# Optimization experiments

Hardware: AMD Instinct MI355X
Metric: run time of the kernel (lower is better)

The kernel has to match this reference:

```python
import jax, jax.numpy as jnp
import numpy as np

D_K = 128
D_V = 128
SEQ_LEN = 2048


def setup_inputs() -> dict:
    key = jax.random.key(0)
    kq, kk, kv = jax.random.split(key, 3)
    q = jax.random.normal(kq, (SEQ_LEN, D_K), dtype=jnp.float32)
    k = jax.random.normal(kk, (SEQ_LEN, D_K), dtype=jnp.float32)
    v = jax.random.normal(kv, (SEQ_LEN, D_V), dtype=jnp.float32)
    return {"q": q, "k": k, "v": v}


def _step(carry, qkv):
    J, Svv, Sqv, Sqq, l = carry
    q, k, v = qkv
    l = l + 1
    fl = l.astype(J.dtype)
    # update_correlations: running means of outer products
    Svv = (fl - 1.0) / fl * Svv + jnp.outer(v, v) / fl
    Sqv = (fl - 1.0) / fl * Sqv + jnp.outer(q, v) / fl
    Sqq = (fl - 1.0) / fl * Sqq + jnp.outer(q, q) / fl

    first = l == 1

    # ecological params (J: [d_v, d_k], Sqv: [d_k, d_v], Sqq: [d_k, d_k])
    s_J = jnp.einsum('vk,kv->', J, Sqv)            # trace(J @ Sigma_qv)
    s_l = k @ Sqv @ v
    A_JJ = jnp.einsum('vk,kj,vj->', J, Sqq, J)     # trace(J Sqq J^T)
    A_ll = (v @ v) * (k @ Sqq @ k)
    A_Jl = v @ J @ Sqq @ k

    # safe denominators (unused branches must not produce NaN under where)
    A_JJ_s = jnp.where(first | (A_JJ == 0), 1.0, A_JJ)
    A_ll_s = jnp.where(first | (A_ll == 0), 1.0, A_ll)
    denom = A_JJ * A_ll - A_Jl ** 2
    denom_s = jnp.where(first | (denom == 0), 1.0, denom)

    margin = s_l - A_Jl * (s_J / A_JJ_s)

    wf = (A_ll * s_J - A_Jl * s_l) / denom_s
    wi = (A_JJ * s_l - A_Jl * s_J) / denom_s
    # nonnegativity constraints (check omega_i first, as in the source)
    wf_c = jnp.where(wi <= 0, s_J / A_JJ_s, jnp.where(wf <= 0, 0.0, wf))
    wi_c = jnp.where(wi <= 0, 0.0, jnp.where(wf <= 0, s_l / A_ll_s, wi))

    do_update = margin > 0
    vk = jnp.outer(v, k)
    J_upd = jnp.where(do_update, wf_c * J + wi_c * vk, J)
    J_new = jnp.where(first, vk, J_upd)
    updated = first | do_update

    # compute_cost with updated J and correlations
    cost = (0.5 * jnp.trace(Svv)
            - jnp.einsum('vk,kv->', J_new, Sqv)
            + 0.5 * jnp.einsum('vk,kj,vj->', J_new, Sqq, J_new))

    return (J_new, Svv, Sqv, Sqq, l), (cost, updated)


def _run(q, k, v):
    d_k, d_v = q.shape[-1], v.shape[-1]
    init = (jnp.zeros((d_v, d_k), q.dtype),
            jnp.zeros((d_v, d_v), q.dtype),
            jnp.zeros((d_k, d_v), q.dtype),
            jnp.zeros((d_k, d_k), q.dtype),
            jnp.int32(0))
    (J, _, _, _, _), (costs, updated) = jax.lax.scan(_step, init, (q, k, v))
    return costs, updated, J


def reference(q, k, v):
    return _run(q, k, v)
```

## Files before the change

kernel.cpp:

```cpp
#include <hip/hip_runtime.h>

#define SEQ 2048
#define D 128

typedef float v2f __attribute__((ext_vector_type(2)));
typedef float v4f __attribute__((ext_vector_type(4)));
#define LO2(v) __builtin_shufflevector(v, v, 0, 1)
#define HI2(v) __builtin_shufflevector(v, v, 2, 3)

__global__ __launch_bounds__(256) void precompute_kernel(
    const float* __restrict__ q, const float* __restrict__ k, const float* __restrict__ v,
    float* __restrict__ U, float* __restrict__ sl, float* __restrict__ kqq,
    float* __restrict__ vv, float* __restrict__ kq_adj, float* __restrict__ vv_adj,
    float* __restrict__ kU_adj, double* __restrict__ invl)
{
    const int s = blockIdx.x;
    const int tid = threadIdx.x;

    __shared__ float ks[D];
    __shared__ float vs[D];
    __shared__ float alpha[SEQ];
    __shared__ float red[8];
    __shared__ float upart[256];

    if (tid < D) ks[tid] = k[s * D + tid];
    else if (tid < 2 * D) vs[tid - D] = v[s * D + (tid - D)];
    __syncthreads();

    float p_a2 = 0.f, p_ab = 0.f;
    for (int i = tid; i <= s; i += 256) {
        const float4* qr = (const float4*)(q + (size_t)i * D);
        const float4* vr = (const float4*)(v + (size_t)i * D);
        float a = 0.f, b = 0.f;
#pragma unroll
        for (int j = 0; j < D / 4; ++j) {
            float4 q4 = qr[j];
            float4 v4 = vr[j];
            a += q4.x * ks[4 * j + 0] + q4.y * ks[4 * j + 1] + q4.z * ks[4 * j + 2] + q4.w * ks[4 * j + 3];
            b += v4.x * vs[4 * j + 0] + v4.y * vs[4 * j + 1] + v4.z * vs[4 * j + 2] + v4.w * vs[4 * j + 3];
        }
        alpha[i] = a;
        p_a2 += a * a;
        p_ab += a * b;
        if (i == s) vv[s] = b;
    }
#pragma unroll
    for (int off = 1; off < 64; off <<= 1) {
        p_a2 += __shfl_xor(p_a2, off);
        p_ab += __shfl_xor(p_ab, off);
    }
    const int wid = tid >> 6;
    if ((tid & 63) == 0) { red[wid] = p_a2; red[4 + wid] = p_ab; }
    __syncthreads();
    if (tid == 0) {
        kqq[s] = red[0] + red[1] + red[2] + red[3];
        sl[s]  = red[4] + red[5] + red[6] + red[7];
        invl[s] = 1.0 / (double)(s + 1);
    }

    if (tid < 64) {
        if (s + 1 < SEQ) {
            float p2 = ks[tid] * q[(size_t)(s + 1) * D + tid]
                     + ks[tid + 64] * q[(size_t)(s + 1) * D + 64 + tid];
#pragma unroll
            for (int off = 1; off < 64; off <<= 1) p2 += __shfl_xor(p2, off);
            if (tid == 0) kq_adj[s + 1] = p2;
        }
        if (s == 0 && tid == 0) { kq_adj[0] = 0.f; kU_adj[0] = 0.f; vv_adj[0] = 0.f; }
    } else if (tid < 128 && s > 0) {
        const int t2 = tid - 64;
        float p2 = vs[t2] * v[(size_t)(s - 1) * D + t2]
                 + vs[t2 + 64] * v[(size_t)(s - 1) * D + 64 + t2];
#pragma unroll
        for (int off = 1; off < 64; off <<= 1) p2 += __shfl_xor(p2, off);
        if (t2 == 0) vv_adj[s] = p2;
    }

    const int c = tid & (D - 1);
    const int h = tid >> 7;
    float a0 = 0.f, a1 = 0.f, a2 = 0.f, a3 = 0.f;
    int i = h;
    for (; i + 6 <= s; i += 8) {
        a0 = fmaf(q[(size_t)(i    ) * D + c], alpha[i    ], a0);
        a1 = fmaf(q[(size_t)(i + 2) * D + c], alpha[i + 2], a1);
        a2 = fmaf(q[(size_t)(i + 4) * D + c], alpha[i + 4], a2);
        a3 = fmaf(q[(size_t)(i + 6) * D + c], alpha[i + 6], a3);
    }
    for (; i <= s; i += 2) a0 = fmaf(q[(size_t)i * D + c], alpha[i], a0);
    upart[tid] = (a0 + a1) + (a2 + a3);
    __syncthreads();

    float kup = 0.f;
    if (tid < D) {
        const float uv = upart[tid] + upart[tid + D];
        U[(size_t)s * D + tid] = uv;
        if (s > 0) kup = uv * k[(size_t)(s - 1) * D + tid];
    }
#pragma unroll
    for (int off = 1; off < 64; off <<= 1) kup += __shfl_xor(kup, off);
    if (tid == 0)  red[0] = kup;
    if (tid == 64) red[1] = kup;
    __syncthreads();
    if (s > 0 && tid == 0) kU_adj[s] = red[0] + red[1];
}

#define DPP_ADD(x, ctrl) \
    ((x) + __int_as_float(__builtin_amdgcn_update_dpp(0, __float_as_int(x), (ctrl), 0xf, 0xf, true)))
#define COMBINE8(x) do { x = DPP_ADD(x, 0xB1); x = DPP_ADD(x, 0x4E); x = DPP_ADD(x, 0x141); } while (0)
#define TAIL3(x)    do { x = DPP_ADD(x, 0x140); x = DPP_ADD(x, 0x142); x = DPP_ADD(x, 0x143); } while (0)
#define REDUCE16(x) do { x = DPP_ADD(x, 0xB1); x = DPP_ADD(x, 0x4E); x = DPP_ADD(x, 0x141); \
                         x = DPP_ADD(x, 0x140); } while (0)

#define UPDATE_J(MODE, WF, WI)                                                \
    if ((MODE) == 2) {                                                        \
        const v2f vc2 = {vcur, vcur};                                         \
        j0 = vc2 * k0_; j1 = vc2 * k1_; j2 = vc2 * k2_; j3 = vc2 * k3_;       \
        j4 = vc2 * k4_; j5 = vc2 * k5_; j6 = vc2 * k6_; j7 = vc2 * k7_;       \
    } else if ((MODE) == 1) {                                                 \
        const v2f wf2 = {(WF), (WF)};                                         \
        const float wvr_ = (WI) * vcur;                                       \
        const v2f wv2 = {wvr_, wvr_};                                         \
        j0 = __builtin_elementwise_fma(j0, wf2, wv2 * k0_);                   \
        j1 = __builtin_elementwise_fma(j1, wf2, wv2 * k1_);                   \
        j2 = __builtin_elementwise_fma(j2, wf2, wv2 * k2_);                   \
        j3 = __builtin_elementwise_fma(j3, wf2, wv2 * k3_);                   \
        j4 = __builtin_elementwise_fma(j4, wf2, wv2 * k4_);                   \
        j5 = __builtin_elementwise_fma(j5, wf2, wv2 * k5_);                   \
        j6 = __builtin_elementwise_fma(j6, wf2, wv2 * k6_);                   \
        j7 = __builtin_elementwise_fma(j7, wf2, wv2 * k7_);                   \
    }

__global__ __launch_bounds__(1024, 4) void scan_kernel(
    const float* __restrict__ q, const float* __restrict__ k, const float* __restrict__ v,
    const float* __restrict__ U, const float* __restrict__ sl_arr,
    const float* __restrict__ kqq_arr, const float* __restrict__ vv_arr,
    const float* __restrict__ kq_adj, const float* __restrict__ vv_adj,
    const float* __restrict__ kU_adj, const double* __restrict__ invl_arr,
    float* __restrict__ out)
{
    const int tid  = threadIdx.x;
    const int lane = tid & 63;
    const int w    = __builtin_amdgcn_readfirstlane(tid >> 6);
    const int r    = tid >> 3;
    const int cg   = tid & 7;
    const int c0s  = cg * 20;

    v2f j0 = {0.f, 0.f}, j1 = j0, j2 = j0, j3 = j0, j4 = j0, j5 = j0, j6 = j0, j7 = j0;

    __shared__ float ring[3][3][160];
    __shared__ __align__(16) float wred[3][16][4];
    __shared__ __align__(16) float decLDS[3][4];

    const bool stager = (tid >= 384) && (tid < 768);
    const int  which  = (tid >> 7) - 3;
    const int  sidx   = tid & 127;
    const int  widx   = ((sidx >> 4) * 20) + (sidx & 15);

    float gstage = 0.f;
    if (stager) {
        if (which == 0) {
            ring[0][0][widx] = q[(size_t)1 * D + sidx];
            ring[1][0][widx] = q[(size_t)2 * D + sidx];
            gstage = q[(size_t)3 * D + sidx];
        } else if (which == 1) {
            ring[0][1][widx] = U[(size_t)1 * D + sidx];
            ring[1][1][widx] = U[(size_t)2 * D + sidx];
            gstage = U[(size_t)3 * D + sidx];
        } else {
            ring[0][2][widx] = k[sidx];
            ring[1][2][widx] = k[(size_t)1 * D + sidx];
            gstage = k[(size_t)2 * D + sidx];
        }
    }
    float vcur = v[r], vnext = v[(size_t)D + r], vn2 = v[(size_t)2 * D + r];

    float dwf = 0.f, dwi = 1.f;
    int dmode = 2;
    if (tid == 0) { decLDS[0][0] = 0.f; decLDS[0][1] = 1.f; decLDS[0][2] = 2.f; decLDS[0][3] = 0.f; }

    double SJ = 0.0, AJJ = 0.0, trSvv = 0.0;
    if (w == 0) {
        const double sl0 = (double)sl_arr[0];
        const double kq0 = (double)kqq_arr[0];
        const double vv0 = (double)vv_arr[0];
        trSvv = vv0;
        SJ  = sl0;
        AJJ = vv0 * kq0;
        if (lane == 0) {
            out[0] = (float)((0.5 * trSvv - SJ + 0.5 * AJJ) * invl_arr[0]);
            out[SEQ] = 1.f;
        }
    }
    __syncthreads();

#define STEP_BODY(I, P, PN, PW)                                               \
{                                                                             \
    float c_sl = 0.f, c_kq = 0.f, c_vv = 0.f, c_kqa = 0.f, c_vva = 0.f,       \
          c_vvp = 0.f, c_kua = 0.f;                                           \
    double c_inv = 0.0;                                                       \
    if (w == 0) {                                                             \
        c_sl  = sl_arr[(I) + 1];  c_kq  = kqq_arr[(I) + 1];                   \
        c_vv  = vv_arr[(I) + 1];  c_kqa = kq_adj[(I) + 1];                    \
        c_vva = vv_adj[(I) + 1];  c_vvp = vv_arr[(I)];                        \
        c_kua = kU_adj[(I) + 1];  c_inv = invl_arr[(I) + 1];                  \
    }                                                                         \
    const v4f Qa = ((const v4f*)&ring[P][0][c0s])[0];                         \
    const v4f Qb = ((const v4f*)&ring[P][0][c0s])[1];                         \
    const v4f Qc = ((const v4f*)&ring[P][0][c0s])[2];                         \
    const v4f Qd = ((const v4f*)&ring[P][0][c0s])[3];                         \
    const v4f Ua = ((const v4f*)&ring[P][1][c0s])[0];                         \
    const v4f Ub = ((const v4f*)&ring[P][1][c0s])[1];                         \
    const v4f Uc = ((const v4f*)&ring[P][1][c0s])[2];                         \
    const v4f Ud = ((const v4f*)&ring[P][1][c0s])[3];                         \
    const v4f Ka = ((const v4f*)&ring[P][2][c0s])[0];                         \
    const v4f Kb = ((const v4f*)&ring[P][2][c0s])[1];                         \
    const v4f Kc = ((const v4f*)&ring[P][2][c0s])[2];                         \
    const v4f Kd = ((const v4f*)&ring[P][2][c0s])[3];                         \
    const v2f k0_ = LO2(Ka), k1_ = HI2(Ka), k2_ = LO2(Kb), k3_ = HI2(Kb);     \
    const v2f k4_ = LO2(Kc), k5_ = HI2(Kc), k6_ = LO2(Kd), k7_ = HI2(Kd);     \
    v2f aq0 = {0.f, 0.f}, aq1 = aq0, aq2 = aq0, aq3 = aq0;                    \
    aq0 = __builtin_elementwise_fma(j0, LO2(Qa), aq0);                        \
    aq1 = __builtin_elementwise_fma(j1, HI2(Qa), aq1);                        \
    aq2 = __builtin_elementwise_fma(j2, LO2(Qb), aq2);                        \
    aq3 = __builtin_elementwise_fma(j3, HI2(Qb), aq3);                        \
    aq0 = __builtin_elementwise_fma(j4, LO2(Qc), aq0);                        \
    aq1 = __builtin_elementwise_fma(j5, HI2(Qc), aq1);                        \
    aq2 = __builtin_elementwise_fma(j6, LO2(Qd), aq2);                        \
    aq3 = __builtin_elementwise_fma(j7, HI2(Qd), aq3);                        \
    const v2f sq_ = (aq0 + aq1) + (aq2 + aq3);                                \
    float Yq = sq_.x + sq_.y;                                                 \
    v2f au0 = {0.f, 0.f}, au1 = au0, au2 = au0, au3 = au0;                    \
    au0 = __builtin_elementwise_fma(j0, LO2(Ua), au0);                        \
    au1 = __builtin_elementwise_fma(j1, HI2(Ua), au1);                        \
    au2 = __builtin_elementwise_fma(j2, LO2(Ub), au2);                        \
    au3 = __builtin_elementwise_fma(j3, HI2(Ub), au3);                        \
    au0 = __builtin_elementwise_fma(j4, LO2(Uc), au0);                        \
    au1 = __builtin_elementwise_fma(j5, HI2(Uc), au1);                        \
    au2 = __builtin_elementwise_fma(j6, LO2(Ud), au2);                        \
    au3 = __builtin_elementwise_fma(j7, HI2(Ud), au3);                        \
    const v2f su_ = (au0 + au1) + (au2 + au3);                                \
    float Yw = su_.x + su_.y;                                                 \
    COMBINE8(Yq);                                                             \
    COMBINE8(Yw);                                                             \
    float z1 = vnext * Yq;                                                    \
    float z2 = Yq * Yq;                                                       \
    float z3 = vcur  * Yq;                                                    \
    float z4 = vnext * Yw;                                                    \
    TAIL3(z1);                                                                \
    TAIL3(z2);                                                                \
    TAIL3(z3);                                                                \
    TAIL3(z4);                                                                \
    if (lane == 63) *(float4*)&wred[P][w][0] = make_float4(z1, z2, z3, z4);   \
    __syncthreads();                                                          \
    if (stager) {                                                             \
        ring[PW][which][widx] = gstage;                                       \
        const int tq_ = ((I) + 4 < SEQ) ? (I) + 4 : SEQ - 1;                  \
        const int tk_ = ((I) + 3 < SEQ) ? (I) + 3 : SEQ - 1;                  \
        gstage = (which == 0) ? q[(size_t)tq_ * D + sidx]                     \
               : (which == 1) ? U[(size_t)tq_ * D + sidx]                     \
                              : k[(size_t)tk_ * D + sidx];                    \
    }                                                                         \
    const int tv_ = ((I) + 3 < SEQ) ? (I) + 3 : SEQ - 1;                      \
    const float vnew_ = v[(size_t)tv_ * D + r];                               \
    if (w == 0) {                                                             \
        float4 ww = *(const float4*)&wred[P][lane & 15][0];                   \
        const float odwf = dwf, odwi = dwi;                                   \
        const int   odmode = dmode;                                           \
        UPDATE_J(odmode, odwf, odwi)                                          \
        REDUCE16(ww.x);                                                       \
        REDUCE16(ww.y);                                                       \
        REDUCE16(ww.z);                                                       \
        REDUCE16(ww.w);                                                       \
        double a_, b_;                                                        \
        if (odmode == 2)      { a_ = 0.0; b_ = 1.0; }                         \
        else if (odmode == 1) { a_ = (double)odwf; b_ = (double)odwi; }       \
        else                  { a_ = 1.0; b_ = 0.0; }                         \
        const double kqa = (double)c_kqa, vva = (double)c_vva;                \
        const double vvp = (double)c_vvp, kua = (double)c_kua;                \
        const double r1 = (double)ww.x * 0.125, r2 = (double)ww.y * 0.125;    \
        const double r3 = (double)ww.z * 0.125, r4 = (double)ww.w * 0.125;    \
        const double Jqv  = a_ * r1 + b_ * (kqa * vva);                       \
        const double Jq2  = a_ * a_ * r2 + 2.0 * a_ * b_ * kqa * r3          \
                          + b_ * b_ * kqa * kqa * vvp;                        \
        const double AJl_ = a_ * r4 + b_ * kua * vva;                         \
        trSvv += (double)c_vv;                                                \
        SJ    += Jqv;                                                         \
        AJJ   += Jq2;                                                         \
        const double s_l  = (double)c_sl;                                     \
        const double A_ll = (double)c_vv * (double)c_kq;                      \
        const double AJJ_s  = (AJJ == 0.0)  ? 1.0 : AJJ;                      \
        const double A_ll_s = (A_ll == 0.0) ? 1.0 : A_ll;                     \
        const double denom   = AJJ * A_ll - AJl_ * AJl_;                      \
        const double denom_s = (denom == 0.0) ? 1.0 : denom;                  \
        const double rden = 1.0 / denom_s;                                    \
        const double wf = (A_ll * SJ - AJl_ * s_l) * rden;                    \
        const double wi = (AJJ * s_l - AJl_ * SJ) * rden;                     \
        double wf_c, wi_c;                                                    \
        if (wi <= 0.0)      { wf_c = SJ / AJJ_s;  wi_c = 0.0; }               \
        else if (wf <= 0.0) { wf_c = 0.0;         wi_c = s_l / A_ll_s; }      \
        else                { wf_c = wf;          wi_c = wi; }                \
        const bool do_update = (s_l * AJJ_s - AJl_ * SJ) > 0.0;               \
        int mode;                                                             \
        if (do_update) {                                                      \
            mode = 1;                                                         \
            const double nSJ = wf_c * SJ + wi_c * s_l;                        \
            AJJ = wf_c * wf_c * AJJ + 2.0 * wf_c * wi_c * AJl_                \
                + wi_c * wi_c * A_ll;                                         \
            SJ = nSJ;                                                         \
        } else {                                                              \
            mode = 0;                                                         \
        }                                                                     \
        dwf = (float)wf_c; dwi = (float)wi_c; dmode = mode;                   \
        if (lane == 0) {                                                      \
            out[(I) + 1] = (float)((0.5 * trSvv - SJ + 0.5 * AJJ) * c_inv);   \
            out[SEQ + (I) + 1] = mode ? 1.f : 0.f;                            \
            *(float4*)&decLDS[PN][0] = make_float4(dwf, dwi, (float)mode, 0.f);\
        }                                                                     \
    } else {                                                                  \
        const float4 df = *(const float4*)&decLDS[P][0];                      \
        dwf = df.x; dwi = df.y; dmode = (int)df.z;                            \
        UPDATE_J(dmode, dwf, dwi)                                             \
    }                                                                         \
    vcur = vnext; vnext = vn2; vn2 = vnew_;                                   \
}

    for (int i = 0; i + 2 < SEQ - 1; i += 3) {
        STEP_BODY(i,     0, 1, 2)
        STEP_BODY(i + 1, 1, 2, 0)
        STEP_BODY(i + 2, 2, 0, 1)
    }
    STEP_BODY(SEQ - 2, 0, 1, 2)
#undef STEP_BODY

    __syncthreads();
    {
        const float4 df = *(const float4*)&decLDS[1][0];
        const float fwf = df.x, fwi = df.y;
        const int   fmode = (int)df.z;
        const v4f Ka = ((const v4f*)&ring[1][2][c0s])[0];
        const v4f Kb = ((const v4f*)&ring[1][2][c0s])[1];
        const v4f Kc = ((const v4f*)&ring[1][2][c0s])[2];
        const v4f Kd = ((const v4f*)&ring[1][2][c0s])[3];
        const v2f k0_ = LO2(Ka), k1_ = HI2(Ka), k2_ = LO2(Kb), k3_ = HI2(Kb);
        const v2f k4_ = LO2(Kc), k5_ = HI2(Kc), k6_ = LO2(Kd), k7_ = HI2(Kd);
        UPDATE_J(fmode, fwf, fwi)
        float* jbase = out + 2 * SEQ + (size_t)r * D + cg * 16;
        *(v4f*)(jbase + 0)  = __builtin_shufflevector(j0, j1, 0, 1, 2, 3);
        *(v4f*)(jbase + 4)  = __builtin_shufflevector(j2, j3, 0, 1, 2, 3);
        *(v4f*)(jbase + 8)  = __builtin_shufflevector(j4, j5, 0, 1, 2, 3);
        *(v4f*)(jbase + 12) = __builtin_shufflevector(j6, j7, 0, 1, 2, 3);
    }
}

extern "C" void kernel_launch(void* const* d_in, const int* in_sizes, int n_in,
                              void* d_out, int out_size, void* d_ws, size_t ws_size,
                              hipStream_t stream) {
    (void)in_sizes; (void)n_in; (void)out_size; (void)ws_size;
    const float* q = (const float*)d_in[0];
    const float* k = (const float*)d_in[1];
    const float* v = (const float*)d_in[2];
    float* out = (float*)d_out;

    float* U      = (float*)d_ws;
    float* sl     = U + (size_t)SEQ * D;
    float* kqq    = sl + SEQ;
    float* vv     = kqq + SEQ;
    float* kq_adj = vv + SEQ;
    float* vv_adj = kq_adj + SEQ;
    float* kU_adj = vv_adj + SEQ;
    double* invl  = (double*)(kU_adj + SEQ);

    precompute_kernel<<<SEQ, 256, 0, stream>>>(q, k, v, U, sl, kqq, vv,
                                               kq_adj, vv_adj, kU_adj, invl);
    scan_kernel<<<1, 1024, 0, stream>>>(q, k, v, U, sl, kqq, vv,
                                        kq_adj, vv_adj, kU_adj, invl, out);
}
```

Before: 2.412 ms.

## Dedicate half the block to J tiles of 4 rows and specialize warps

Reassigns the J matrix so only the upper 8 warps hold it, each thread owning a 4-row by 8-column tile, instead of all 16 warps holding an 8x16 strip. Warp 0 no longer holds J and only does the scalar decision logic. The other warps stage q, U, k and v into a shared ring, with v now staged via LDS too. This shortens the per-step reduction (16-lane DPP instead of 64-lane) and reduces LDS traffic per J element, but concentrates J FMA work on fewer threads and changes the partial-sum layout and scaling.

```diff
diff --git a/kernel.cpp b/kernel.cpp
--- a/kernel.cpp
+++ b/kernel.cpp
@@ -106,28 +106,38 @@
 
 #define DPP_ADD(x, ctrl) \
     ((x) + __int_as_float(__builtin_amdgcn_update_dpp(0, __float_as_int(x), (ctrl), 0xf, 0xf, true)))
-#define COMBINE8(x) do { x = DPP_ADD(x, 0xB1); x = DPP_ADD(x, 0x4E); x = DPP_ADD(x, 0x141); } while (0)
-#define TAIL3(x)    do { x = DPP_ADD(x, 0x140); x = DPP_ADD(x, 0x142); x = DPP_ADD(x, 0x143); } while (0)
-#define REDUCE16(x) do { x = DPP_ADD(x, 0xB1); x = DPP_ADD(x, 0x4E); x = DPP_ADD(x, 0x141); \
-                         x = DPP_ADD(x, 0x140); } while (0)
+#define REDUCE16(x) do { x = DPP_ADD(x, 0xB1); x = DPP_ADD(x, 0x4E); \
+                         x = DPP_ADD(x, 0x141); x = DPP_ADD(x, 0x140); } while (0)
 
 #define UPDATE_J(MODE, WF, WI)                                                \
     if ((MODE) == 2) {                                                        \
-        const v2f vc2 = {vcur, vcur};                                         \
-        j0 = vc2 * k0_; j1 = vc2 * k1_; j2 = vc2 * k2_; j3 = vc2 * k3_;       \
-        j4 = vc2 * k4_; j5 = vc2 * k5_; j6 = vc2 * k6_; j7 = vc2 * k7_;       \
+        const v2f wA = {vc4.x, vc4.x}, wB = {vc4.y, vc4.y};                   \
+        const v2f wC = {vc4.z, vc4.z}, wD = {vc4.w, vc4.w};                   \
+        jA0 = wA * k0_; jA1 = wA * k1_; jA2 = wA * k2_; jA3 = wA * k3_;       \
+        jB0 = wB * k0_; jB1 = wB * k1_; jB2 = wB * k2_; jB3 = wB * k3_;       \
+        jC0 = wC * k0_; jC1 = wC * k1_; jC2 = wC * k2_; jC3 = wC * k3_;       \
+        jD0 = wD * k0_; jD1 = wD * k1_; jD2 = wD * k2_; jD3 = wD * k3_;       \
     } else if ((MODE) == 1) {                                                 \
         const v2f wf2 = {(WF), (WF)};                                         \
-        const float wvr_ = (WI) * vcur;                                       \
-        const v2f wv2 = {wvr_, wvr_};                                         \
-        j0 = __builtin_elementwise_fma(j0, wf2, wv2 * k0_);                   \
-        j1 = __builtin_elementwise_fma(j1, wf2, wv2 * k1_);                   \
-        j2 = __builtin_elementwise_fma(j2, wf2, wv2 * k2_);                   \
-        j3 = __builtin_elementwise_fma(j3, wf2, wv2 * k3_);                   \
-        j4 = __builtin_elementwise_fma(j4, wf2, wv2 * k4_);                   \
-        j5 = __builtin_elementwise_fma(j5, wf2, wv2 * k5_);                   \
-        j6 = __builtin_elementwise_fma(j6, wf2, wv2 * k6_);                   \
-        j7 = __builtin_elementwise_fma(j7, wf2, wv2 * k7_);                   \
+        const float sA = (WI) * vc4.x, sB = (WI) * vc4.y;                     \
+        const float sC = (WI) * vc4.z, sD = (WI) * vc4.w;                     \
+        const v2f wA = {sA, sA}, wB = {sB, sB}, wC = {sC, sC}, wD = {sD, sD}; \
+        jA0 = __builtin_elementwise_fma(jA0, wf2, wA * k0_);                  \
+        jA1 = __builtin_elementwise_fma(jA1, wf2, wA * k1_);                  \
+        jA2 = __builtin_elementwise_fma(jA2, wf2, wA * k2_);                  \
+        jA3 = __builtin_elementwise_fma(jA3, wf2, wA * k3_);                  \
+        jB0 = __builtin_elementwise_fma(jB0, wf2, wB * k0_);                  \
+        jB1 = __builtin_elementwise_fma(jB1, wf2, wB * k1_);                  \
+        jB2 = __builtin_elementwise_fma(jB2, wf2, wB * k2_);                  \
+        jB3 = __builtin_elementwise_fma(jB3, wf2, wB * k3_);                  \
+        jC0 = __builtin_elementwise_fma(jC0, wf2, wC * k0_);                  \
+        jC1 = __builtin_elementwise_fma(jC1, wf2, wC * k1_);                  \
+        jC2 = __builtin_elementwise_fma(jC2, wf2, wC * k2_);                  \
+        jC3 = __builtin_elementwise_fma(jC3, wf2, wC * k3_);                  \
+        jD0 = __builtin_elementwise_fma(jD0, wf2, wD * k0_);                  \
+        jD1 = __builtin_elementwise_fma(jD1, wf2, wD * k1_);                  \
+        jD2 = __builtin_elementwise_fma(jD2, wf2, wD * k2_);                  \
+        jD3 = __builtin_elementwise_fma(jD3, wf2, wD * k3_);                  \
     }
 
 __global__ __launch_bounds__(1024, 4) void scan_kernel(
@@ -141,22 +151,37 @@
     const int tid  = threadIdx.x;
     const int lane = tid & 63;
     const int w    = __builtin_amdgcn_readfirstlane(tid >> 6);
-    const int r    = tid >> 3;
-    const int cg   = tid & 7;
-    const int c0s  = cg * 20;
-
-    v2f j0 = {0.f, 0.f}, j1 = j0, j2 = j0, j3 = j0, j4 = j0, j5 = j0, j6 = j0, j7 = j0;
-
-    __shared__ float ring[3][3][160];
-    __shared__ __align__(16) float wred[3][16][4];
+
+    __shared__ float ring[3][4][160];
+    __shared__ __align__(16) float wred[3][32][4];
     __shared__ __align__(16) float decLDS[3][4];
 
-    const bool stager = (tid >= 384) && (tid < 768);
-    const int  which  = (tid >> 7) - 3;
-    const int  sidx   = tid & 127;
-    const int  widx   = ((sidx >> 4) * 20) + (sidx & 15);
+    const bool isj     = (tid >= 512);
+    const int  jw      = w - 8;
+    const int  i16     = lane & 15;
+    const int  r4      = lane >> 4;
+    const int  o       = 20 * (i16 >> 1) + 8 * (i16 & 1);
+    const int  rb      = (jw << 4) + (r4 << 2);
+    const int  vo      = 20 * jw + (r4 << 2);
+
+    const bool stager  = (tid >= 128) && (tid < 512);
+    const int  which   = (tid >> 7) - 1;
+    const int  sidx    = tid & 127;
+    const int  widx    = ((sidx >> 4) * 20) + (sidx & 15);
+
+    const bool vstager = (tid >= 64) && (tid < 128);
+    const int  s2      = tid & 63;
+    const int  vc0     = 2 * s2;
+    const int  vwidx   = 20 * (vc0 >> 4) + (vc0 & 15);
+
+    v2f jA0 = {0.f, 0.f}, jA1 = jA0, jA2 = jA0, jA3 = jA0;
+    v2f jB0 = jA0, jB1 = jA0, jB2 = jA0, jB3 = jA0;
+    v2f jC0 = jA0, jC1 = jA0, jC2 = jA0, jC3 = jA0;
+    v2f jD0 = jA0, jD1 = jA0, jD2 = jA0, jD3 = jA0;
+    v4f vc4 = {0.f, 0.f, 0.f, 0.f}, vn4 = vc4;
 
     float gstage = 0.f;
+    v2f   gv = {0.f, 0.f};
     if (stager) {
         if (which == 0) {
             ring[0][0][widx] = q[(size_t)1 * D + sidx];
@@ -171,8 +196,13 @@
             ring[1][2][widx] = k[(size_t)1 * D + sidx];
             gstage = k[(size_t)2 * D + sidx];
         }
-    }
-    float vcur = v[r], vnext = v[(size_t)D + r], vn2 = v[(size_t)2 * D + r];
+    } else if (vstager) {
+        *(v2f*)&ring[0][3][vwidx] = *(const v2f*)&v[(size_t)1 * D + vc0];
+        *(v2f*)&ring[1][3][vwidx] = *(const v2f*)&v[(size_t)2 * D + vc0];
+        gv = *(const v2f*)&v[(size_t)3 * D + vc0];
+    } else if (isj) {
+        vc4 = *(const v4f*)&v[rb];
+    }
 
     float dwf = 0.f, dwi = 1.f;
     int dmode = 2;
@@ -204,53 +234,53 @@
         c_vva = vv_adj[(I) + 1];  c_vvp = vv_arr[(I)];                        \
         c_kua = kU_adj[(I) + 1];  c_inv = invl_arr[(I) + 1];                  \
     }                                                                         \
-    const v4f Qa = ((const v4f*)&ring[P][0][c0s])[0];                         \
-    const v4f Qb = ((const v4f*)&ring[P][0][c0s])[1];                         \
-    const v4f Qc = ((const v4f*)&ring[P][0][c0s])[2];                         \
-    const v4f Qd = ((const v4f*)&ring[P][0][c0s])[3];                         \
-    const v4f Ua = ((const v4f*)&ring[P][1][c0s])[0];                         \
-    const v4f Ub = ((const v4f*)&ring[P][1][c0s])[1];                         \
-    const v4f Uc = ((const v4f*)&ring[P][1][c0s])[2];                         \
-    const v4f Ud = ((const v4f*)&ring[P][1][c0s])[3];                         \
-    const v4f Ka = ((const v4f*)&ring[P][2][c0s])[0];                         \
-    const v4f Kb = ((const v4f*)&ring[P][2][c0s])[1];                         \
-    const v4f Kc = ((const v4f*)&ring[P][2][c0s])[2];                         \
-    const v4f Kd = ((const v4f*)&ring[P][2][c0s])[3];                         \
-    const v2f k0_ = LO2(Ka), k1_ = HI2(Ka), k2_ = LO2(Kb), k3_ = HI2(Kb);     \
-    const v2f k4_ = LO2(Kc), k5_ = HI2(Kc), k6_ = LO2(Kd), k7_ = HI2(Kd);     \
-    v2f aq0 = {0.f, 0.f}, aq1 = aq0, aq2 = aq0, aq3 = aq0;                    \
-    aq0 = __builtin_elementwise_fma(j0, LO2(Qa), aq0);                        \
-    aq1 = __builtin_elementwise_fma(j1, HI2(Qa), aq1);                        \
-    aq2 = __builtin_elementwise_fma(j2, LO2(Qb), aq2);                        \
-    aq3 = __builtin_elementwise_fma(j3, HI2(Qb), aq3);                        \
-    aq0 = __builtin_elementwise_fma(j4, LO2(Qc), aq0);                        \
-    aq1 = __builtin_elementwise_fma(j5, HI2(Qc), aq1);                        \
-    aq2 = __builtin_elementwise_fma(j6, LO2(Qd), aq2);                        \
-    aq3 = __builtin_elementwise_fma(j7, HI2(Qd), aq3);                        \
-    const v2f sq_ = (aq0 + aq1) + (aq2 + aq3);                                \
-    float Yq = sq_.x + sq_.y;                                                 \
-    v2f au0 = {0.f, 0.f}, au1 = au0, au2 = au0, au3 = au0;                    \
-    au0 = __builtin_elementwise_fma(j0, LO2(Ua), au0);                        \
-    au1 = __builtin_elementwise_fma(j1, HI2(Ua), au1);                        \
-    au2 = __builtin_elementwise_fma(j2, LO2(Ub), au2);                        \
-    au3 = __builtin_elementwise_fma(j3, HI2(Ub), au3);                        \
-    au0 = __builtin_elementwise_fma(j4, LO2(Uc), au0);                        \
-    au1 = __builtin_elementwise_fma(j5, HI2(Uc), au1);                        \
-    au2 = __builtin_elementwise_fma(j6, LO2(Ud), au2);                        \
-    au3 = __builtin_elementwise_fma(j7, HI2(Ud), au3);                        \
-    const v2f su_ = (au0 + au1) + (au2 + au3);                                \
-    float Yw = su_.x + su_.y;                                                 \
-    COMBINE8(Yq);                                                             \
-    COMBINE8(Yw);                                                             \
-    float z1 = vnext * Yq;                                                    \
-    float z2 = Yq * Yq;                                                       \
-    float z3 = vcur  * Yq;                                                    \
-    float z4 = vnext * Yw;                                                    \
-    TAIL3(z1);                                                                \
-    TAIL3(z2);                                                                \
-    TAIL3(z3);                                                                \
-    TAIL3(z4);                                                                \
-    if (lane == 63) *(float4*)&wred[P][w][0] = make_float4(z1, z2, z3, z4);   \
+    if (isj) {                                                                \
+        const v4f Qa = ((const v4f*)&ring[P][0][o])[0];                       \
+        const v4f Qb = ((const v4f*)&ring[P][0][o])[1];                       \
+        const v4f Ua = ((const v4f*)&ring[P][1][o])[0];                       \
+        const v4f Ub = ((const v4f*)&ring[P][1][o])[1];                       \
+        vn4 = *((const v4f*)&ring[P][3][vo]);                                 \
+        const v2f q0 = LO2(Qa), q1 = HI2(Qa), q2 = LO2(Qb), q3 = HI2(Qb);     \
+        v2f aA = jA0 * q0, aB = jB0 * q0, aC = jC0 * q0, aD = jD0 * q0;       \
+        aA = __builtin_elementwise_fma(jA1, q1, aA);                          \
+        aB = __builtin_elementwise_fma(jB1, q1, aB);                          \
+        aC = __builtin_elementwise_fma(jC1, q1, aC);                          \
+        aD = __builtin_elementwise_fma(jD1, q1, aD);                          \
+        aA = __builtin_elementwise_fma(jA2, q2, aA);                          \
+        aB = __builtin_elementwise_fma(jB2, q2, aB);                          \
+        aC = __builtin_elementwise_fma(jC2, q2, aC);                          \
+        aD = __builtin_elementwise_fma(jD2, q2, aD);                          \
+        aA = __builtin_elementwise_fma(jA3, q3, aA);                          \
+        aB = __builtin_elementwise_fma(jB3, q3, aB);                          \
+        aC = __builtin_elementwise_fma(jC3, q3, aC);                          \
+        aD = __builtin_elementwise_fma(jD3, q3, aD);                          \
+        float YqA = aA.x + aA.y, YqB = aB.x + aB.y;                           \
+        float YqC = aC.x + aC.y, YqD = aD.x + aD.y;                           \
+        const v2f u0 = LO2(Ua), u1 = HI2(Ua), u2 = LO2(Ub), u3 = HI2(Ub);     \
+        v2f bA = jA0 * u0, bB = jB0 * u0, bC = jC0 * u0, bD = jD0 * u0;       \
+        bA = __builtin_elementwise_fma(jA1, u1, bA);                          \
+        bB = __builtin_elementwise_fma(jB1, u1, bB);                          \
+        bC = __builtin_elementwise_fma(jC1, u1, bC);                          \
+        bD = __builtin_elementwise_fma(jD1, u1, bD);                          \
+        bA = __builtin_elementwise_fma(jA2, u2, bA);                          \
+        bB = __builtin_elementwise_fma(jB2, u2, bB);                          \
+        bC = __builtin_elementwise_fma(jC2, u2, bC);                          \
+        bD = __builtin_elementwise_fma(jD2, u2, bD);                          \
+        bA = __builtin_elementwise_fma(jA3, u3, bA);                          \
+        bB = __builtin_elementwise_fma(jB3, u3, bB);                          \
+        bC = __builtin_elementwise_fma(jC3, u3, bC);                          \
+        bD = __builtin_elementwise_fma(jD3, u3, bD);                          \
+        float YwA = bA.x + bA.y, YwB = bB.x + bB.y;                           \
+        float YwC = bC.x + bC.y, YwD = bD.x + bD.y;                           \
+        REDUCE16(YqA); REDUCE16(YqB); REDUCE16(YqC); REDUCE16(YqD);           \
+        REDUCE16(YwA); REDUCE16(YwB); REDUCE16(YwC); REDUCE16(YwD);           \
+        const float z1 = (vn4.x * YqA + vn4.y * YqB) + (vn4.z * YqC + vn4.w * YqD); \
+        const float z2 = (YqA * YqA + YqB * YqB) + (YqC * YqC + YqD * YqD);   \
+        const float z3 = (vc4.x * YqA + vc4.y * YqB) + (vc4.z * YqC + vc4.w * YqD); \
+        const float z4 = (vn4.x * YwA + vn4.y * YwB) + (vn4.z * YwC + vn4.w * YwD); \
+        if ((lane & 15) == 15)                                                \
+            *(float4*)&wred[P][(jw << 2) | r4][0] = make_float4(z1, z2, z3, z4); \
+    }                                                                         \
     __syncthreads();                                                          \
     if (stager) {                                                             \
         ring[PW][which][widx] = gstage;                                       \
@@ -259,14 +289,26 @@
         gstage = (which == 0) ? q[(size_t)tq_ * D + sidx]                     \
                : (which == 1) ? U[(size_t)tq_ * D + sidx]                     \
                               : k[(size_t)tk_ * D + sidx];                    \
-    }                                                                         \
-    const int tv_ = ((I) + 3 < SEQ) ? (I) + 3 : SEQ - 1;                      \
-    const float vnew_ = v[(size_t)tv_ * D + r];                               \
-    if (w == 0) {                                                             \
-        float4 ww = *(const float4*)&wred[P][lane & 15][0];                   \
+    } else if (vstager) {                                                     \
+        *(v2f*)&ring[PW][3][vwidx] = gv;                                      \
+        const int tv_ = ((I) + 4 < SEQ) ? (I) + 4 : SEQ - 1;                  \
+        gv = *(const v2f*)&v[(size_t)tv_ * D + vc0];                          \
+    } else if (isj) {                                                         \
+        const float4 df = *(const float4*)&decLDS[P][0];                      \
+        const v4f Ka = ((const v4f*)&ring[P][2][o])[0];                       \
+        const v4f Kb = ((const v4f*)&ring[P][2][o])[1];                       \
+        const v2f k0_ = LO2(Ka), k1_ = HI2(Ka), k2_ = LO2(Kb), k3_ = HI2(Kb); \
+        const float uwf = df.x, uwi = df.y;                                   \
+        const int   umode = (int)df.z;                                        \
+        UPDATE_J(umode, uwf, uwi)                                             \
+        vc4 = vn4;                                                            \
+    } else if (w == 0) {                                                      \
+        const float4 wa = *(const float4*)&wred[P][lane & 15][0];             \
+        const float4 wb = *(const float4*)&wred[P][16 + (lane & 15)][0];      \
+        float4 ww = make_float4(wa.x + wb.x, wa.y + wb.y,                     \
+                                wa.z + wb.z, wa.w + wb.w);                    \
         const float odwf = dwf, odwi = dwi;                                   \
         const int   odmode = dmode;                                           \
-        UPDATE_J(odmode, odwf, odwi)                                          \
         REDUCE16(ww.x);                                                       \
         REDUCE16(ww.y);                                                       \
         REDUCE16(ww.z);                                                       \
@@ -277,12 +319,12 @@
         else                  { a_ = 1.0; b_ = 0.0; }                         \
         const double kqa = (double)c_kqa, vva = (double)c_vva;                \
         const double vvp = (double)c_vvp, kua = (double)c_kua;                \
-        const double r1 = (double)ww.x * 0.125, r2 = (double)ww.y * 0.125;    \
-        const double r3 = (double)ww.z * 0.125, r4 = (double)ww.w * 0.125;    \
+        const double r1 = (double)ww.x, r2 = (double)ww.y;                    \
+        const double r3 = (double)ww.z, r4_ = (double)ww.w;                   \
         const double Jqv  = a_ * r1 + b_ * (kqa * vva);                       \
         const double Jq2  = a_ * a_ * r2 + 2.0 * a_ * b_ * kqa * r3          \
                           + b_ * b_ * kqa * kqa * vvp;                        \
-        const double AJl_ = a_ * r4 + b_ * kua * vva;                         \
+        const double AJl_ = a_ * r4_ + b_ * kua * vva;                        \
         trSvv += (double)c_vv;                                                \
         SJ    += Jqv;                                                         \
         AJJ   += Jq2;                                                         \
@@ -316,12 +358,7 @@
             out[SEQ + (I) + 1] = mode ? 1.f : 0.f;                            \
             *(float4*)&decLDS[PN][0] = make_float4(dwf, dwi, (float)mode, 0.f);\
         }                                                                     \
-    } else {                                                                  \
-        const float4 df = *(const float4*)&decLDS[P][0];                      \
-        dwf = df.x; dwi = df.y; dmode = (int)df.z;                            \
-        UPDATE_J(dmode, dwf, dwi)                                             \
     }                                                                         \
-    vcur = vnext; vnext = vn2; vn2 = vnew_;                                   \
 }
 
     for (int i = 0; i + 2 < SEQ - 1; i += 3) {
@@ -333,22 +370,23 @@
 #undef STEP_BODY
 
     __syncthreads();
-    {
+    if (isj) {
         const float4 df = *(const float4*)&decLDS[1][0];
         const float fwf = df.x, fwi = df.y;
         const int   fmode = (int)df.z;
-        const v4f Ka = ((const v4f*)&ring[1][2][c0s])[0];
-        const v4f Kb = ((const v4f*)&ring[1][2][c0s])[1];
-        const v4f Kc = ((const v4f*)&ring[1][2][c0s])[2];
-        const v4f Kd = ((const v4f*)&ring[1][2][c0s])[3];
+        const v4f Ka = ((const v4f*)&ring[1][2][o])[0];
+        const v4f Kb = ((const v4f*)&ring[1][2][o])[1];
         const v2f k0_ = LO2(Ka), k1_ = HI2(Ka), k2_ = LO2(Kb), k3_ = HI2(Kb);
-        const v2f k4_ = LO2(Kc), k5_ = HI2(Kc), k6_ = LO2(Kd), k7_ = HI2(Kd);
         UPDATE_J(fmode, fwf, fwi)
-        float* jbase = out + 2 * SEQ + (size_t)r * D + cg * 16;
-        *(v4f*)(jbase + 0)  = __builtin_shufflevector(j0, j1, 0, 1, 2, 3);
-        *(v4f*)(jbase + 4)  = __builtin_shufflevector(j2, j3, 0, 1, 2, 3);
-        *(v4f*)(jbase + 8)  = __builtin_shufflevector(j4, j5, 0, 1, 2, 3);
-        *(v4f*)(jbase + 12) = __builtin_shufflevector(j6, j7, 0, 1, 2, 3);
+        float* jb = out + 2 * SEQ + (size_t)rb * D + 8 * i16;
+        *(v4f*)(jb + 0)         = __builtin_shufflevector(jA0, jA1, 0, 1, 2, 3);
+        *(v4f*)(jb + 4)         = __builtin_shufflevector(jA2, jA3, 0, 1, 2, 3);
+        *(v4f*)(jb + D + 0)     = __builtin_shufflevector(jB0, jB1, 0, 1, 2, 3);
+        *(v4f*)(jb + D + 4)     = __builtin_shufflevector(jB2, jB3, 0, 1, 2, 3);
+        *(v4f*)(jb + 2 * D + 0) = __builtin_shufflevector(jC0, jC1, 0, 1, 2, 3);
+        *(v4f*)(jb + 2 * D + 4) = __builtin_shufflevector(jC2, jC3, 0, 1, 2, 3);
+        *(v4f*)(jb + 3 * D + 0) = __builtin_shufflevector(jD0, jD1, 0, 1, 2, 3);
+        *(v4f*)(jb + 3 * D + 4) = __builtin_shufflevector(jD2, jD3, 0, 1, 2, 3);
     }
 }
 
```

Result: slower. 2.533 ms (+5.0%).

## Fuse precompute and scan into one kernel with per-step flag gating

Applied to the files above, without the earlier changes.

Merges the precompute kernel and the sequential scan kernel into one launch. Block 0 runs the scan while the other blocks compute per-step quantities and publish per-step ready flags with release stores. The scan polls those flags in windows ahead of the step it is on, so precompute overlaps with the serial scan instead of finishing first. Precompute blocks grow from 256 to 1024 threads. The design relies on block 0 being scheduled alongside the producer blocks, adds spin-wait and fence overhead, and adds a memset of the flags.

```diff
diff --git a/kernel.cpp b/kernel.cpp
--- a/kernel.cpp
+++ b/kernel.cpp
@@ -7,102 +7,6 @@
 typedef float v4f __attribute__((ext_vector_type(4)));
 #define LO2(v) __builtin_shufflevector(v, v, 0, 1)
 #define HI2(v) __builtin_shufflevector(v, v, 2, 3)
-
-__global__ __launch_bounds__(256) void precompute_kernel(
-    const float* __restrict__ q, const float* __restrict__ k, const float* __restrict__ v,
-    float* __restrict__ U, float* __restrict__ sl, float* __restrict__ kqq,
-    float* __restrict__ vv, float* __restrict__ kq_adj, float* __restrict__ vv_adj,
-    float* __restrict__ kU_adj, double* __restrict__ invl)
-{
-    const int s = blockIdx.x;
-    const int tid = threadIdx.x;
-
-    __shared__ float ks[D];
-    __shared__ float vs[D];
-    __shared__ float alpha[SEQ];
-    __shared__ float red[8];
-    __shared__ float upart[256];
-
-    if (tid < D) ks[tid] = k[s * D + tid];
-    else if (tid < 2 * D) vs[tid - D] = v[s * D + (tid - D)];
-    __syncthreads();
-
-    float p_a2 = 0.f, p_ab = 0.f;
-    for (int i = tid; i <= s; i += 256) {
-        const float4* qr = (const float4*)(q + (size_t)i * D);
-        const float4* vr = (const float4*)(v + (size_t)i * D);
-        float a = 0.f, b = 0.f;
-#pragma unroll
-        for (int j = 0; j < D / 4; ++j) {
-            float4 q4 = qr[j];
-            float4 v4 = vr[j];
-            a += q4.x * ks[4 * j + 0] + q4.y * ks[4 * j + 1] + q4.z * ks[4 * j + 2] + q4.w * ks[4 * j + 3];
-            b += v4.x * vs[4 * j + 0] + v4.y * vs[4 * j + 1] + v4.z * vs[4 * j + 2] + v4.w * vs[4 * j + 3];
-        }
-        alpha[i] = a;
-        p_a2 += a * a;
-        p_ab += a * b;
-        if (i == s) vv[s] = b;
-    }
-#pragma unroll
-    for (int off = 1; off < 64; off <<= 1) {
-        p_a2 += __shfl_xor(p_a2, off);
-        p_ab += __shfl_xor(p_ab, off);
-    }
-    const int wid = tid >> 6;
-    if ((tid & 63) == 0) { red[wid] = p_a2; red[4 + wid] = p_ab; }
-    __syncthreads();
-    if (tid == 0) {
-        kqq[s] = red[0] + red[1] + red[2] + red[3];
-        sl[s]  = red[4] + red[5] + red[6] + red[7];
-        invl[s] = 1.0 / (double)(s + 1);
-    }
-
-    if (tid < 64) {
-        if (s + 1 < SEQ) {
-            float p2 = ks[tid] * q[(size_t)(s + 1) * D + tid]
-                     + ks[tid + 64] * q[(size_t)(s + 1) * D + 64 + tid];
-#pragma unroll
-            for (int off = 1; off < 64; off <<= 1) p2 += __shfl_xor(p2, off);
-            if (tid == 0) kq_adj[s + 1] = p2;
-        }
-        if (s == 0 && tid == 0) { kq_adj[0] = 0.f; kU_adj[0] = 0.f; vv_adj[0] = 0.f; }
-    } else if (tid < 128 && s > 0) {
-        const int t2 = tid - 64;
-        float p2 = vs[t2] * v[(size_t)(s - 1) * D + t2]
-                 + vs[t2 + 64] * v[(size_t)(s - 1) * D + 64 + t2];
-#pragma unroll
-        for (int off = 1; off < 64; off <<= 1) p2 += __shfl_xor(p2, off);
-        if (t2 == 0) vv_adj[s] = p2;
-    }
-
-    const int c = tid & (D - 1);
-    const int h = tid >> 7;
-    float a0 = 0.f, a1 = 0.f, a2 = 0.f, a3 = 0.f;
-    int i = h;
-    for (; i + 6 <= s; i += 8) {
-        a0 = fmaf(q[(size_t)(i    ) * D + c], alpha[i    ], a0);
-        a1 = fmaf(q[(size_t)(i + 2) * D + c], alpha[i + 2], a1);
-        a2 = fmaf(q[(size_t)(i + 4) * D + c], alpha[i + 4], a2);
-        a3 = fmaf(q[(size_t)(i + 6) * D + c], alpha[i + 6], a3);
-    }
-    for (; i <= s; i += 2) a0 = fmaf(q[(size_t)i * D + c], alpha[i], a0);
-    upart[tid] = (a0 + a1) + (a2 + a3);
-    __syncthreads();
-
-    float kup = 0.f;
-    if (tid < D) {
-        const float uv = upart[tid] + upart[tid + D];
-        U[(size_t)s * D + tid] = uv;
-        if (s > 0) kup = uv * k[(size_t)(s - 1) * D + tid];
-    }
-#pragma unroll
-    for (int off = 1; off < 64; off <<= 1) kup += __shfl_xor(kup, off);
-    if (tid == 0)  red[0] = kup;
-    if (tid == 64) red[1] = kup;
-    __syncthreads();
-    if (s > 0 && tid == 0) kU_adj[s] = red[0] + red[1];
-}
 
 #define DPP_ADD(x, ctrl) \
     ((x) + __int_as_float(__builtin_amdgcn_update_dpp(0, __float_as_int(x), (ctrl), 0xf, 0xf, true)))
@@ -130,16 +34,133 @@
         j7 = __builtin_elementwise_fma(j7, wf2, wv2 * k7_);                   \
     }
 
-__global__ __launch_bounds__(1024, 4) void scan_kernel(
+__global__ __launch_bounds__(1024, 2) void fused_kernel(
     const float* __restrict__ q, const float* __restrict__ k, const float* __restrict__ v,
-    const float* __restrict__ U, const float* __restrict__ sl_arr,
-    const float* __restrict__ kqq_arr, const float* __restrict__ vv_arr,
-    const float* __restrict__ kq_adj, const float* __restrict__ vv_adj,
-    const float* __restrict__ kU_adj, const double* __restrict__ invl_arr,
-    float* __restrict__ out)
+    float* __restrict__ U, float* __restrict__ sl_arr,
+    float* __restrict__ kqq_arr, float* __restrict__ vv_arr,
+    float* __restrict__ kq_adj, float* __restrict__ vv_adj,
+    float* __restrict__ kU_adj, double* __restrict__ invl_arr,
+    float* __restrict__ out, int* flags)
 {
     const int tid  = threadIdx.x;
     const int lane = tid & 63;
+
+    if (blockIdx.x != 0) {
+        const int s = blockIdx.x - 1;
+
+        __shared__ float ks[D];
+        __shared__ float vs[D];
+        __shared__ float alpha[SEQ];
+        __shared__ float red[32];
+        __shared__ float upart[1024];
+
+        if (tid < D) ks[tid] = k[s * D + tid];
+        else if (tid < 2 * D) vs[tid - D] = v[s * D + (tid - D)];
+        __syncthreads();
+
+        float p_a2 = 0.f, p_ab = 0.f;
+        for (int i = tid; i <= s; i += 1024) {
+            const float4* qr = (const float4*)(q + (size_t)i * D);
+            const float4* vr = (const float4*)(v + (size_t)i * D);
+            float a = 0.f, b = 0.f;
+#pragma unroll
+            for (int j = 0; j < D / 4; ++j) {
+                float4 q4 = qr[j];
+                float4 v4 = vr[j];
+                a += q4.x * ks[4 * j + 0] + q4.y * ks[4 * j + 1] + q4.z * ks[4 * j + 2] + q4.w * ks[4 * j + 3];
+                b += v4.x * vs[4 * j + 0] + v4.y * vs[4 * j + 1] + v4.z * vs[4 * j + 2] + v4.w * vs[4 * j + 3];
+            }
+            alpha[i] = a;
+            p_a2 += a * a;
+            p_ab += a * b;
+            if (i == s) vv_arr[s] = b;
+        }
+#pragma unroll
+        for (int off = 1; off < 64; off <<= 1) {
+            p_a2 += __shfl_xor(p_a2, off);
+            p_ab += __shfl_xor(p_ab, off);
+        }
+        const int wid = tid >> 6;
+        if ((tid & 63) == 0) { red[wid] = p_a2; red[16 + wid] = p_ab; }
+        __syncthreads();
+        if (tid == 0) {
+            float s1 = 0.f, s2 = 0.f;
+#pragma unroll
+            for (int j = 0; j < 16; ++j) { s1 += red[j]; s2 += red[16 + j]; }
+            kqq_arr[s] = s1;
+            sl_arr[s]  = s2;
+            invl_arr[s] = 1.0 / (double)(s + 1);
+        }
+
+        if (tid < 64) {
+            if (s + 1 < SEQ) {
+                float p2 = ks[tid] * q[(size_t)(s + 1) * D + tid]
+                         + ks[tid + 64] * q[(size_t)(s + 1) * D + 64 + tid];
+#pragma unroll
+                for (int off = 1; off < 64; off <<= 1) p2 += __shfl_xor(p2, off);
+                if (tid == 0) kq_adj[s + 1] = p2;
+            }
+            if (s == 0 && tid == 0) { kq_adj[0] = 0.f; kU_adj[0] = 0.f; vv_adj[0] = 0.f; }
+        } else if (tid < 128 && s > 0) {
+            const int t2 = tid - 64;
+            float p2 = vs[t2] * v[(size_t)(s - 1) * D + t2]
+                     + vs[t2 + 64] * v[(size_t)(s - 1) * D + 64 + t2];
+#pragma unroll
+            for (int off = 1; off < 64; off <<= 1) p2 += __shfl_xor(p2, off);
+            if (t2 == 0) vv_adj[s] = p2;
+        }
+
+        const int c = tid & (D - 1);
+        const int h = tid >> 7;
+        float a0 = 0.f, a1 = 0.f, a2 = 0.f, a3 = 0.f;
+        int i = h;
+        for (; i + 24 <= s; i += 32) {
+            a0 = fmaf(q[(size_t)(i     ) * D + c], alpha[i     ], a0);
+            a1 = fmaf(q[(size_t)(i +  8) * D + c], alpha[i +  8], a1);
+            a2 = fmaf(q[(size_t)(i + 16) * D + c], alpha[i + 16], a2);
+            a3 = fmaf(q[(size_t)(i + 24) * D + c], alpha[i + 24], a3);
+        }
+        for (; i <= s; i += 8) a0 = fmaf(q[(size_t)i * D + c], alpha[i], a0);
+        upart[tid] = (a0 + a1) + (a2 + a3);
+        __syncthreads();
+
+        float kup = 0.f;
+        if (tid < D) {
+            float uv = 0.f;
+#pragma unroll
+            for (int j = 0; j < 8; ++j) uv += upart[tid + 128 * j];
+            U[(size_t)s * D + tid] = uv;
+            if (s > 0) kup = uv * k[(size_t)(s - 1) * D + tid];
+        }
+#pragma unroll
+        for (int off = 1; off < 64; off <<= 1) kup += __shfl_xor(kup, off);
+        if (tid == 0)  red[0] = kup;
+        if (tid == 64) red[1] = kup;
+        __syncthreads();
+        if (s > 0 && tid == 0) kU_adj[s] = red[0] + red[1];
+
+        __syncthreads();
+        __threadfence();
+        if (tid == 0)
+            __hip_atomic_store(&flags[s], 1, __ATOMIC_RELEASE, __HIP_MEMORY_SCOPE_AGENT);
+        return;
+    }
+
+#define WAITGATE(T)                                                           \
+    {                                                                         \
+        int t_ = (T); if (t_ > SEQ - 1) t_ = SEQ - 1;                         \
+        int i0_ = t_ - 127; if (i0_ < 0) i0_ = 0;                             \
+        const int a_ = i0_ + lane; const int b_ = a_ + 64;                    \
+        for (;;) {                                                            \
+            int fa_ = (a_ <= t_) ? __hip_atomic_load(&flags[a_],              \
+                        __ATOMIC_ACQUIRE, __HIP_MEMORY_SCOPE_AGENT) : 1;      \
+            int fb_ = (b_ <= t_) ? __hip_atomic_load(&flags[b_],              \
+                        __ATOMIC_ACQUIRE, __HIP_MEMORY_SCOPE_AGENT) : 1;      \
+            if (__all(fa_ && fb_)) break;                                     \
+            __builtin_amdgcn_s_sleep(8);                                      \
+        }                                                                     \
+    }
+
     const int w    = __builtin_amdgcn_readfirstlane(tid >> 6);
     const int r    = tid >> 3;
     const int cg   = tid & 7;
@@ -155,6 +176,8 @@
     const int  which  = (tid >> 7) - 3;
     const int  sidx   = tid & 127;
     const int  widx   = ((sidx >> 4) * 20) + (sidx & 15);
+
+    WAITGATE(99)
 
     float gstage = 0.f;
     if (stager) {
@@ -325,12 +348,14 @@
 }
 
     for (int i = 0; i + 2 < SEQ - 1; i += 3) {
+        if (i && (i % 96) == 0) WAITGATE(i + 99)
         STEP_BODY(i,     0, 1, 2)
         STEP_BODY(i + 1, 1, 2, 0)
         STEP_BODY(i + 2, 2, 0, 1)
     }
     STEP_BODY(SEQ - 2, 0, 1, 2)
 #undef STEP_BODY
+#undef WAITGATE
 
     __syncthreads();
     {
@@ -369,9 +394,10 @@
     float* vv_adj = kq_adj + SEQ;
     float* kU_adj = vv_adj + SEQ;
     double* invl  = (double*)(kU_adj + SEQ);
-
-    precompute_kernel<<<SEQ, 256, 0, stream>>>(q, k, v, U, sl, kqq, vv,
-                                               kq_adj, vv_adj, kU_adj, invl);
-    scan_kernel<<<1, 1024, 0, stream>>>(q, k, v, U, sl, kqq, vv,
-                                        kq_adj, vv_adj, kU_adj, invl, out);
+    int*    flags = (int*)(invl + SEQ);
+
+    hipMemsetAsync(flags, 0, SEQ * sizeof(int), stream);
+    fused_kernel<<<SEQ + 1, 1024, 0, stream>>>(q, k, v, U, sl, kqq, vv,
+                                               kq_adj, vv_adj, kU_adj, invl,
+                                               out, flags);
 }
```

Measured after the change: 3.032 ms. +25.7%, slower.
